# Optimization experiments

Hardware: AMD Instinct MI355X
Metric: run time of the kernel (lower is better)

Reference implementation:

```python
import jax, jax.numpy as jnp
import numpy as np

# Model constants (match init_kwargs config)
D_MODEL, D_INNER, D_HEAD, N_HEADS = 1024, 2048, 64, 32
D_STATE, D_CONV, CHUNK, N_LAYERS = 64, 4, 256, 2
CONV_DIM = D_INNER + 2 * D_STATE        # n_groups = 1
D_IN_PROJ = 2 * D_INNER + 2 * D_STATE + N_HEADS
B_SZ, L_SEQ = 2, 4096
EPS = 1e-5


def setup_inputs() -> dict:
    key = jax.random.key(0)
    ks = jax.random.split(key, 8)
    x = jax.random.normal(ks[0], (B_SZ, L_SEQ, D_MODEL), jnp.float32)
    in_proj_w = jax.random.normal(ks[1], (N_LAYERS, D_IN_PROJ, D_MODEL), jnp.float32) * 0.02
    conv_w = jax.random.normal(ks[2], (N_LAYERS, CONV_DIM, D_CONV), jnp.float32) * 0.2
    conv_b = jax.random.normal(ks[3], (N_LAYERS, CONV_DIM), jnp.float32) * 0.02
    # dt_bias init as in the torch code: inverse-softplus of dt ~ LogUniform(1e-3, 1e-1)
    dt = jnp.exp(jax.random.uniform(ks[4], (N_LAYERS, N_HEADS))
                 * (np.log(0.1) - np.log(0.001)) + np.log(0.001))
    dt = jnp.clip(dt, 1e-4, None)
    dt_bias = dt + jnp.log(-jnp.expm1(-dt))
    A_log = jnp.log(jax.random.uniform(ks[5], (N_LAYERS, N_HEADS), minval=1.0, maxval=16.0))
    D = jnp.ones((N_LAYERS, N_HEADS), jnp.float32)
    gnorm_w = jnp.ones((N_LAYERS, D_INNER), jnp.float32)
    out_proj_w = jax.random.normal(ks[6], (N_LAYERS, D_MODEL, D_INNER), jnp.float32) * 0.02
    norm_w = jnp.ones((N_LAYERS, D_MODEL), jnp.float32)
    return dict(x=x, in_proj_w=in_proj_w, conv_w=conv_w, conv_b=conv_b, dt_bias=dt_bias,
                A_log=A_log, D=D, gnorm_w=gnorm_w, out_proj_w=out_proj_w, norm_w=norm_w)


def _rmsnorm(x, w, eps=EPS):
    return x * jax.lax.rsqrt(jnp.mean(x * x, axis=-1, keepdims=True) + eps) * w


def _segsum(x):
    # x: (..., T) -> (..., T, T) with S[i, j] = sum_{j < k <= i} x[k], -inf above diag
    T = x.shape[-1]
    cs = jnp.cumsum(x, axis=-1)
    d = cs[..., :, None] - cs[..., None, :]
    return jnp.where(jnp.tril(jnp.ones((T, T), bool)), d, -jnp.inf)


def _causal_conv1d(x, w, b):
    # depthwise causal conv: x (B,L,C), w (C,K), b (C)
    K = w.shape[-1]
    L = x.shape[1]
    xp = jnp.pad(x, ((0, 0), (K - 1, 0), (0, 0)))
    out = jnp.broadcast_to(b, x.shape)
    for i in range(K):
        out = out + xp[:, i:i + L, :] * w[:, i]
    return out


def _ssd(X, dt, A, B, C, D):
    # Exact chunked SSD scan (mamba_chunk_scan_combined), n_groups=1.
    # X (b,l,h,p), dt (b,l,h), A (h), B,C (b,l,n)
    b, l, h, p = X.shape
    n = B.shape[-1]
    nc = l // CHUNK
    Xdt = X * dt[..., None]
    dA = (dt * A).reshape(b, nc, CHUNK, h).transpose(0, 3, 1, 2)     # (b,h,z,c)
    dAcs = jnp.cumsum(dA, axis=-1)
    Lmat = jnp.exp(_segsum(dA))                                      # (b,h,z,c,c)
    Bc = B.reshape(b, nc, CHUNK, n)
    Cc = C.reshape(b, nc, CHUNK, n)
    Xc = Xdt.reshape(b, nc, CHUNK, h, p)
    # intra-chunk (diagonal) part
    G = jnp.einsum('bzln,bzsn->bzls', Cc, Bc)                        # (b,z,c,c)
    M = G[:, None] * Lmat                                            # (b,h,z,c,c)
    Yd = jnp.einsum('bhzls,bzshp->bzlhp', M, Xc)
    # chunk states
    decay_states = jnp.exp(dAcs[..., -1:] - dAcs)                    # (b,h,z,c)
    states = jnp.einsum('bzln,bhzl,bzlhp->bzhpn', Bc, decay_states, Xc)
    # inter-chunk recurrence
    chunk_decay = jnp.exp(_segsum(jnp.pad(dAcs[..., -1], ((0, 0), (0, 0), (1, 0)))))
    states0 = jnp.concatenate([jnp.zeros_like(states[:, :1]), states], axis=1)
    prev = jnp.einsum('bhzc,bchpn->bzhpn', chunk_decay, states0)[:, :-1]
    Yo = jnp.einsum('bzln,bzhpn,bhzl->bzlhp', Cc, prev, jnp.exp(dAcs))
    Y = (Yd + Yo).reshape(b, l, h, p) + X * D[None, None, :, None]
    return Y


def _block(x, in_w, cw, cb, dtb, a_log, d_skip, gw, ow, nw):
    b, l, _ = x.shape
    h = _rmsnorm(x, nw)
    zxbcdt = jnp.einsum('bld,ed->ble', h, in_w)
    z = zxbcdt[..., :D_INNER]
    xBC = zxbcdt[..., D_INNER:D_INNER + CONV_DIM]
    dt = jax.nn.softplus(zxbcdt[..., D_INNER + CONV_DIM:] + dtb)      # (b,l,H)
    xBC = jax.nn.silu(_causal_conv1d(xBC, cw, cb))
    xs = xBC[..., :D_INNER].reshape(b, l, N_HEADS, D_HEAD)
    Bm = xBC[..., D_INNER:D_INNER + D_STATE]
    Cm = xBC[..., D_INNER + D_STATE:]
    A = -jnp.exp(a_log)
    y = _ssd(xs, dt, A, Bm, Cm, d_skip).reshape(b, l, D_INNER)
    y = _rmsnorm(y * jax.nn.silu(z), gw)                              # gated RMSNorm (gate before norm)
    return x + jnp.einsum('bli,di->bld', y, ow)


def reference(x, in_proj_w, conv_w, conv_b, dt_bias, A_log, D, gnorm_w, out_proj_w, norm_w):
    for i in range(in_proj_w.shape[0]):
        x = _block(x, in_proj_w[i], conv_w[i], conv_b[i], dt_bias[i],
                   A_log[i], D[i], gnorm_w[i], out_proj_w[i], norm_w[i])
    return x
```

## Files before the change

kernel.cpp:

```cpp
#include <hip/hip_runtime.h>

#define DMODEL   1024
#define DINNER   2048
#define NHEADS   32
#define DHEAD    64
#define DSTATE   64
#define CONVDIM  2176
#define DINPROJ  4256
#define LSEQ     4096
#define BSZ      2
#define NCHUNK   16
#define CHUNK    256
#define NROWS    8192
#define NPAD     4352
#define XT_P     264
#define M_P      40

typedef __attribute__((ext_vector_type(8))) short  short8;
typedef __attribute__((ext_vector_type(4))) float  f32x4;
typedef __attribute__((ext_vector_type(4))) unsigned short us4;

__device__ __forceinline__ float bf2f(unsigned short u){
  return __uint_as_float(((unsigned int)u) << 16);
}
__device__ __forceinline__ unsigned short f2bf(float f){
  unsigned int i = __float_as_uint(f);
  i += 0x7fffu + ((i >> 16) & 1u);
  return (unsigned short)(i >> 16);
}

__device__ __forceinline__ void gl_lds16(const void* g, void* l){
  __builtin_amdgcn_global_load_lds(
      (const __attribute__((address_space(1))) unsigned int*)g,
      (__attribute__((address_space(3))) unsigned int*)l, 16, 0, 0);
}

__global__ void cast_pad_kernel(const float* __restrict__ src, unsigned short* __restrict__ dst,
                                int rows_src, int cols, long long total){
  long long i = (long long)blockIdx.x * 256 + threadIdx.x;
  if (i >= total) return;
  long long r = i / cols;
  dst[i] = (r < rows_src) ? f2bf(src[i]) : (unsigned short)0;
}

__global__ void rmsnorm_kernel(const float* __restrict__ x, const float* __restrict__ w,
                               unsigned short* __restrict__ out){
  int r = blockIdx.x, t = threadIdx.x;
  const float* xr = x + (size_t)r * DMODEL;
  float v[4]; float s = 0.f;
#pragma unroll
  for (int i = 0; i < 4; ++i){ v[i] = xr[t + i*256]; s += v[i]*v[i]; }
  __shared__ float red[4];
  for (int off = 32; off; off >>= 1) s += __shfl_down(s, off, 64);
  if ((t & 63) == 0) red[t >> 6] = s;
  __syncthreads();
  s = red[0] + red[1] + red[2] + red[3];
  float sc = rsqrtf(s * (1.f/DMODEL) + 1e-5f);
#pragma unroll
  for (int i = 0; i < 4; ++i)
    out[(size_t)r*DMODEL + t + i*256] = f2bf(v[i]*sc*w[t + i*256]);
}

template<int EPI>
__launch_bounds__(256, 2)
__global__ void gemm_bt(const unsigned short* __restrict__ A, const unsigned short* __restrict__ Bw,
                        void* __restrict__ Cout, const float* __restrict__ Cres,
                        int K, int Nstore){
  __shared__ __align__(16) unsigned short As[128*64];
  __shared__ __align__(16) unsigned short Bs[128*64];
  const int m0 = blockIdx.y * 128, n0 = blockIdx.x * 128;
  const int t = threadIdx.x, w = t >> 6, lane = t & 63;
  const int wr = w >> 1, wc = w & 1;
  const int srow = lane >> 3;
  const int scol = (lane & 7) * 8;
  f32x4 acc[4][4] = {};

  for (int k0 = 0; k0 < K; k0 += 64){
#pragma unroll
    for (int it = 0; it < 4; ++it){
      int rr = (w*4 + it)*8 + srow;
      gl_lds16(A  + (size_t)(m0 + rr)*K + k0 + scol, &As[(w*4 + it)*512]);
      gl_lds16(Bw + (size_t)(n0 + rr)*K + k0 + scol, &Bs[(w*4 + it)*512]);
    }
    __syncthreads();
#pragma unroll
    for (int kk = 0; kk < 64; kk += 32){
      short8 af[4], bfr[4];
      int col = kk + (lane >> 4)*8;
#pragma unroll
      for (int m = 0; m < 4; ++m)
        af[m] = *(const short8*)&As[(wr*64 + m*16 + (lane & 15))*64 + col];
#pragma unroll
      for (int n = 0; n < 4; ++n)
        bfr[n] = *(const short8*)&Bs[(wc*64 + n*16 + (lane & 15))*64 + col];
#pragma unroll
      for (int m = 0; m < 4; ++m)
#pragma unroll
        for (int n = 0; n < 4; ++n)
          acc[m][n] = __builtin_amdgcn_mfma_f32_16x16x32_bf16(af[m], bfr[n], acc[m][n], 0, 0, 0);
    }
    __syncthreads();
  }

#pragma unroll
  for (int m = 0; m < 4; ++m){
#pragma unroll
    for (int n = 0; n < 4; ++n){
      int col = n0 + wc*64 + n*16 + (lane & 15);
      if (col < Nstore){
#pragma unroll
        for (int r = 0; r < 4; ++r){
          int row = m0 + wr*64 + m*16 + (lane >> 4)*4 + r;
          if (EPI == 0)
            ((unsigned short*)Cout)[(size_t)row*Nstore + col] = f2bf(acc[m][n][r]);
          else
            ((float*)Cout)[(size_t)row*Nstore + col] =
                Cres[(size_t)row*Nstore + col] + acc[m][n][r];
        }
      }
    }
  }
}

__global__ void conv_silu_kernel(const unsigned short* __restrict__ zx,
                                 const float* __restrict__ cw, const float* __restrict__ cb,
                                 unsigned short* __restrict__ X, unsigned short* __restrict__ Bm,
                                 unsigned short* __restrict__ Cm){
  int c = blockIdx.x * 256 + threadIdx.x;
  if (c >= CONVDIM) return;
  int r = blockIdx.y;
  int l = r & (LSEQ - 1);
  float acc = cb[c];
  float w0 = cw[c*4+0], w1 = cw[c*4+1], w2 = cw[c*4+2], w3 = cw[c*4+3];
#pragma unroll
  for (int i = 0; i < 4; ++i){
    int li = l - 3 + i;
    if (li >= 0){
      float v = bf2f(zx[(size_t)(r - 3 + i)*DINPROJ + DINNER + c]);
      float wi = (i==0)?w0:(i==1)?w1:(i==2)?w2:w3;
      acc += v * wi;
    }
  }
  float s = acc / (1.f + __expf(-acc));
  if (c < DINNER)            X[(size_t)r*DINNER + c]        = f2bf(s);
  else if (c < DINNER+DSTATE) Bm[(size_t)r*DSTATE + c-DINNER] = f2bf(s);
  else                        Cm[(size_t)r*DSTATE + c-DINNER-DSTATE] = f2bf(s);
}

__global__ void dtscan_kernel(const unsigned short* __restrict__ zx, const float* __restrict__ dtb,
                              const float* __restrict__ A_log,
                              float* __restrict__ dt_sp, float* __restrict__ dAcs_g){
  const int z = blockIdx.x, hh = blockIdx.y, b = blockIdx.z;
  const int t = threadIdx.x;
  __shared__ float sdA[CHUNK];
  const float Ah = -__expf(A_log[hh]);
  size_t r = (size_t)b*LSEQ + z*CHUNK + t;
  float raw = bf2f(zx[r*DINPROJ + DINNER + CONVDIM + hh]) + dtb[hh];
  float dtv = raw > 20.f ? raw : log1pf(__expf(raw));
  sdA[t] = dtv * Ah;
  __syncthreads();
  for (int off = 1; off < CHUNK; off <<= 1){
    float v = (t >= off) ? sdA[t - off] : 0.f;
    __syncthreads();
    sdA[t] += v;
    __syncthreads();
  }
  size_t hb = (size_t)(b*NHEADS + hh);
  dt_sp[hb*LSEQ + z*CHUNK + t] = dtv;
  dAcs_g[(hb*NCHUNK + z)*CHUNK + t] = sdA[t];
}

__launch_bounds__(256, 2)
__global__ void chunk_main_kernel(const unsigned short* __restrict__ X,
                                  const unsigned short* __restrict__ Bm,
                                  const unsigned short* __restrict__ Cm,
                                  const float* __restrict__ dt_sp,
                                  const float* __restrict__ dAcs_g,
                                  float* __restrict__ states,
                                  unsigned short* __restrict__ Yb){
  const int z = blockIdx.x, hh = blockIdx.y, b = blockIdx.z;
  const int t = threadIdx.x, w = t >> 6, lane = t & 63;
  __shared__ __align__(16) unsigned short Xt[64 * XT_P];
  __shared__ __align__(16) unsigned short U[64 * XT_P];
  __shared__ float sdA[CHUNK];
  __shared__ float sdt[CHUNK];

  const size_t row0 = (size_t)b*LSEQ + z*CHUNK;
  const size_t hb = (size_t)(b*NHEADS + hh);
  sdA[t] = dAcs_g[(hb*NCHUNK + z)*CHUNK + t];
  sdt[t] = dt_sp[hb*LSEQ + z*CHUNK + t];
  __syncthreads();
  const float total = sdA[CHUNK-1];

  for (int it = 0; it < 16; ++it){
    int l = it*16 + (t >> 4);
    int p4 = (t & 15) * 4;
    float dtl = sdt[l];
    float dec = __expf(total - sdA[l]);
    us4 xv = *(const us4*)(X  + (row0 + l)*DINNER + hh*DHEAD + p4);
    us4 bv = *(const us4*)(Bm + (row0 + l)*DSTATE + p4);
#pragma unroll
    for (int j = 0; j < 4; ++j){
      Xt[(p4 + j)*XT_P + l] = f2bf(bf2f(xv[j]) * dtl);
      U [(p4 + j)*XT_P + l] = f2bf(bf2f(bv[j]) * dec);
    }
  }
  __syncthreads();

  {
    f32x4 sacc[4] = {};
    for (int k2 = 0; k2 < 8; ++k2){
      int kc = k2*32 + (lane >> 4)*8;
      short8 a = *(const short8*)&U[(w*16 + (lane & 15))*XT_P + kc];
#pragma unroll
      for (int pt = 0; pt < 4; ++pt){
        short8 bfr = *(const short8*)&Xt[(pt*16 + (lane & 15))*XT_P + kc];
        sacc[pt] = __builtin_amdgcn_mfma_f32_16x16x32_bf16(a, bfr, sacc[pt], 0, 0, 0);
      }
    }
    float* sp = states + (((size_t)b*NCHUNK + z)*NHEADS + hh)*(DHEAD*DSTATE);
#pragma unroll
    for (int pt = 0; pt < 4; ++pt){
      int p = pt*16 + (lane & 15);
#pragma unroll
      for (int r = 0; r < 4; ++r){
        int n = w*16 + (lane >> 4)*4 + r;
        sp[p*DSTATE + n] = sacc[pt][r];
      }
    }
  }
  __syncthreads();

  unsigned short* Mw = U + w * (64 * M_P);
  short8 cfr[4][2];
#pragma unroll
  for (int lt = 0; lt < 4; ++lt){
    int lg = w + lt*4;
#pragma unroll
    for (int k2 = 0; k2 < 2; ++k2)
      cfr[lt][k2] = *(const short8*)(Cm + (row0 + lg*16 + (lane & 15))*DSTATE + k2*32 + (lane >> 4)*8);
  }
  f32x4 yacc[4][4] = {};
  for (int st = 0; st < 8; ++st){
    short8 gb[2][2];
#pragma unroll
    for (int ss = 0; ss < 2; ++ss)
#pragma unroll
      for (int k2 = 0; k2 < 2; ++k2)
        gb[ss][k2] = *(const short8*)(Bm + (row0 + st*32 + ss*16 + (lane & 15))*DSTATE + k2*32 + (lane >> 4)*8);
    short8 xb[4];
#pragma unroll
    for (int pt = 0; pt < 4; ++pt)
      xb[pt] = *(const short8*)&Xt[(pt*16 + (lane & 15))*XT_P + st*32 + (lane >> 4)*8];
#pragma unroll
    for (int lt = 0; lt < 4; ++lt){
      int lg = w + lt*4;
      if (st*32 > lg*16 + 15) continue;
#pragma unroll
      for (int ss = 0; ss < 2; ++ss){
        f32x4 g = {};
        g = __builtin_amdgcn_mfma_f32_16x16x32_bf16(cfr[lt][0], gb[ss][0], g, 0, 0, 0);
        g = __builtin_amdgcn_mfma_f32_16x16x32_bf16(cfr[lt][1], gb[ss][1], g, 0, 0, 0);
        int s = st*32 + ss*16 + (lane & 15);
        float sdAs = sdA[s];
#pragma unroll
        for (int r = 0; r < 4; ++r){
          int l = lg*16 + (lane >> 4)*4 + r;
          float m = (s <= l) ? __expf(sdA[l] - sdAs) : 0.f;
          Mw[(lt*16 + (lane >> 4)*4 + r)*M_P + ss*16 + (lane & 15)] = f2bf(g[r] * m);
        }
      }
      short8 mf = *(const short8*)&Mw[(lt*16 + (lane & 15))*M_P + (lane >> 4)*8];
#pragma unroll
      for (int pt = 0; pt < 4; ++pt)
        yacc[lt][pt] = __builtin_amdgcn_mfma_f32_16x16x32_bf16(mf, xb[pt], yacc[lt][pt], 0, 0, 0);
    }
  }
  __syncthreads();

  unsigned short* Yst = U + w * 4096;
#pragma unroll
  for (int lt = 0; lt < 4; ++lt)
#pragma unroll
    for (int pt = 0; pt < 4; ++pt)
#pragma unroll
      for (int r = 0; r < 4; ++r){
        int row = lt*16 + (lane >> 4)*4 + r;
        int c = pt*16 + (lane & 15);
        int cs = (c & 7) | ((((c >> 3) ^ (row & 7)) & 7) << 3);
        Yst[row*64 + cs] = f2bf(yacc[lt][pt][r]);
      }
  __syncthreads();
  {
    int ltl = lane >> 4, rr = lane & 15;
    int row = ltl*16 + rr;
    int lg = (w + ltl*4)*16 + rr;
    unsigned short* dst = Yb + (row0 + lg)*DINNER + hh*DHEAD;
#pragma unroll
    for (int k = 0; k < 8; ++k){
      short8 v = *(const short8*)&Yst[row*64 + ((k ^ (row & 7)) << 3)];
      *(short8*)(dst + k*8) = v;
    }
  }
}

__launch_bounds__(64)
__global__ void state_recur_kernel(const float* __restrict__ states, const float* __restrict__ dAcs_g,
                                   unsigned short* __restrict__ prev_bf){
  const int hh = blockIdx.x, b = blockIdx.y, t = threadIdx.x;
  float S[64];
#pragma unroll
  for (int j = 0; j < 64; ++j) S[j] = 0.f;
  for (int z = 0; z < NCHUNK; ++z){
    size_t idx = (((size_t)b*NCHUNK + z)*NHEADS + hh)*(DHEAD*DSTATE) + (size_t)t*DSTATE;
    float cd = __expf(dAcs_g[(((size_t)(b*NHEADS + hh))*NCHUNK + z)*CHUNK + CHUNK-1]);
    const float* st = states + idx;
    unsigned short* pb = prev_bf + idx;
#pragma unroll
    for (int j = 0; j < 64; ++j){
      pb[j] = f2bf(S[j]);
      S[j] = S[j]*cd + st[j];
    }
  }
}

__launch_bounds__(256, 2)
__global__ void chunk_out_kernel(const unsigned short* __restrict__ X,
                                 const unsigned short* __restrict__ Cm,
                                 const float* __restrict__ dAcs_g, const unsigned short* __restrict__ prev_bf,
                                 const float* __restrict__ Dp, unsigned short* __restrict__ Yb){
  const int z = blockIdx.x, hh = blockIdx.y, b = blockIdx.z;
  const int t = threadIdx.x, w = t >> 6, lane = t & 63;
  __shared__ __align__(16) float Yo[4][64*64];
  __shared__ float sdA[CHUNK];
  const size_t row0 = (size_t)b*LSEQ + z*CHUNK;
  sdA[t] = dAcs_g[(((size_t)(b*NHEADS + hh))*NCHUNK + z)*CHUNK + t];
  __syncthreads();
  const unsigned short* pvb = prev_bf + (((size_t)b*NCHUNK + z)*NHEADS + hh)*(DHEAD*DSTATE);
  const float Dh = Dp[hh];

  f32x4 acc[4][4] = {};
#pragma unroll
  for (int k2 = 0; k2 < 2; ++k2){
    int kc = k2*32 + (lane >> 4)*8;
    short8 a[4], bfr[4];
#pragma unroll
    for (int lt = 0; lt < 4; ++lt)
      a[lt] = *(const short8*)(Cm + (row0 + w*64 + lt*16 + (lane & 15))*DSTATE + kc);
#pragma unroll
    for (int pt = 0; pt < 4; ++pt)
      bfr[pt] = *(const short8*)(pvb + (size_t)(pt*16 + (lane & 15))*DSTATE + kc);
#pragma unroll
    for (int lt = 0; lt < 4; ++lt)
#pragma unroll
      for (int pt = 0; pt < 4; ++pt)
        acc[lt][pt] = __builtin_amdgcn_mfma_f32_16x16x32_bf16(a[lt], bfr[pt], acc[lt][pt], 0, 0, 0);
  }

#pragma unroll
  for (int lt = 0; lt < 4; ++lt){
    float eA[4];
#pragma unroll
    for (int r = 0; r < 4; ++r)
      eA[r] = __expf(sdA[w*64 + lt*16 + (lane >> 4)*4 + r]);
#pragma unroll
    for (int pt = 0; pt < 4; ++pt){
      int c = pt*16 + (lane & 15);
#pragma unroll
      for (int r = 0; r < 4; ++r){
        int row = lt*16 + (lane >> 4)*4 + r;
        int blk = ((c >> 2) ^ (row & 15)) & 15;
        Yo[w][row*64 + (c & 3) + (blk << 2)] = acc[lt][pt][r] * eA[r];
      }
    }
  }
  __syncthreads();
  {
    int l = w*64 + lane;
    const unsigned short* xr = X + (row0 + l)*DINNER + hh*DHEAD;
    unsigned short* yr = Yb + (row0 + l)*DINNER + hh*DHEAD;
#pragma unroll
    for (int k = 0; k < 16; ++k){
      f32x4 v = *(const f32x4*)&Yo[w][lane*64 + (((k ^ (lane & 15)) & 15) << 2)];
      us4 yb = *(const us4*)(yr + k*4);
      us4 xv = *(const us4*)(xr + k*4);
      us4 o;
#pragma unroll
      for (int j = 0; j < 4; ++j)
        o[j] = f2bf(bf2f(yb[j]) + v[j] + Dh*bf2f(xv[j]));
      *(us4*)(yr + k*4) = o;
    }
  }
}

__global__ void gated_rmsnorm_kernel(const unsigned short* __restrict__ Yb,
                                     const unsigned short* __restrict__ zx,
                                     const float* __restrict__ gw, unsigned short* __restrict__ out){
  int r = blockIdx.x, t = threadIdx.x;
  float vals[8]; float s = 0.f;
#pragma unroll
  for (int i = 0; i < 8; ++i){
    int c = t + i*256;
    float y  = bf2f(Yb[(size_t)r*DINNER + c]);
    float zv = bf2f(zx[(size_t)r*DINPROJ + c]);
    float g  = y * (zv / (1.f + __expf(-zv)));
    vals[i] = g; s += g*g;
  }
  __shared__ float red[4];
  for (int off = 32; off; off >>= 1) s += __shfl_down(s, off, 64);
  if ((t & 63) == 0) red[t >> 6] = s;
  __syncthreads();
  s = red[0] + red[1] + red[2] + red[3];
  float sc = rsqrtf(s * (1.f/DINNER) + 1e-5f);
#pragma unroll
  for (int i = 0; i < 8; ++i)
    out[(size_t)r*DINNER + t + i*256] = f2bf(vals[i]*sc*gw[t + i*256]);
}

extern "C" void kernel_launch(void* const* d_in, const int* in_sizes, int n_in,
                              void* d_out, int out_size, void* d_ws, size_t ws_size,
                              hipStream_t stream){
  const float* x      = (const float*)d_in[0];
  const float* in_w   = (const float*)d_in[1];
  const float* conv_w = (const float*)d_in[2];
  const float* conv_b = (const float*)d_in[3];
  const float* dt_b   = (const float*)d_in[4];
  const float* A_log  = (const float*)d_in[5];
  const float* Dp     = (const float*)d_in[6];
  const float* gnw    = (const float*)d_in[7];
  const float* out_w  = (const float*)d_in[8];
  const float* norm_w = (const float*)d_in[9];
  float* outp = (float*)d_out;

  const size_t NEEDED =
      (size_t)NROWS*DMODEL*2 + (size_t)NPAD*DMODEL*2 + (size_t)DMODEL*DINNER*2
    + (size_t)NROWS*DINPROJ*2 + (size_t)NROWS*DINNER*2  + (size_t)NROWS*DINNER*2
    + (size_t)NROWS*DSTATE*2*2 + (size_t)BSZ*NHEADS*LSEQ*4
    + (size_t)BSZ*NHEADS*NCHUNK*CHUNK*4
    + (size_t)BSZ*NCHUNK*NHEADS*DHEAD*DSTATE*4
    + (size_t)BSZ*NCHUNK*NHEADS*DHEAD*DSTATE*2
    + 40*256;
  if (ws_size < NEEDED) return;

  char* p = (char*)d_ws;
  auto alloc = [&](size_t n){ char* r = p; p += (n + 255) & ~(size_t)255; return (void*)r; };
  unsigned short* h    = (unsigned short*)alloc((size_t)NROWS*DMODEL*2);
  unsigned short* wA   = (unsigned short*)alloc((size_t)NPAD*DMODEL*2);
  unsigned short* wO   = (unsigned short*)alloc((size_t)DMODEL*DINNER*2);
  unsigned short* zx   = (unsigned short*)alloc((size_t)NROWS*DINPROJ*2);
  unsigned short* X    = (unsigned short*)alloc((size_t)NROWS*DINNER*2);
  unsigned short* Yb   = (unsigned short*)alloc((size_t)NROWS*DINNER*2);
  unsigned short* Bm   = (unsigned short*)alloc((size_t)NROWS*DSTATE*2);
  unsigned short* Cm   = (unsigned short*)alloc((size_t)NROWS*DSTATE*2);
  float* dtbuf  = (float*)alloc((size_t)BSZ*NHEADS*LSEQ*4);
  float* dAcs   = (float*)alloc((size_t)BSZ*NHEADS*NCHUNK*CHUNK*4);
  float* states = (float*)alloc((size_t)BSZ*NCHUNK*NHEADS*DHEAD*DSTATE*4);
  unsigned short* prev_bf = (unsigned short*)alloc((size_t)BSZ*NCHUNK*NHEADS*DHEAD*DSTATE*2);
  unsigned short* yn = X;

  for (int layer = 0; layer < 2; ++layer){
    const float* xprev = (layer == 0) ? x : outp;
    float* xnext = outp;

    cast_pad_kernel<<<(NPAD*DMODEL + 255)/256, 256, 0, stream>>>(
        in_w + (size_t)layer*DINPROJ*DMODEL, wA, DINPROJ, DMODEL, (long long)NPAD*DMODEL);
    rmsnorm_kernel<<<NROWS, 256, 0, stream>>>(xprev, norm_w + layer*DMODEL, h);
    gemm_bt<0><<<dim3(NPAD/128, NROWS/128), 256, 0, stream>>>(
        h, wA, (void*)zx, nullptr, DMODEL, DINPROJ);
    conv_silu_kernel<<<dim3((CONVDIM + 255)/256, NROWS), 256, 0, stream>>>(
        zx, conv_w + (size_t)layer*CONVDIM*4, conv_b + layer*CONVDIM, X, Bm, Cm);
    dtscan_kernel<<<dim3(NCHUNK, NHEADS, BSZ), 256, 0, stream>>>(
        zx, dt_b + layer*NHEADS, A_log + layer*NHEADS, dtbuf, dAcs);
    chunk_main_kernel<<<dim3(NCHUNK, NHEADS, BSZ), 256, 0, stream>>>(
        X, Bm, Cm, dtbuf, dAcs, states, Yb);
    state_recur_kernel<<<dim3(NHEADS, BSZ), 64, 0, stream>>>(states, dAcs, prev_bf);
    chunk_out_kernel<<<dim3(NCHUNK, NHEADS, BSZ), 256, 0, stream>>>(
        X, Cm, dAcs, prev_bf, Dp + layer*NHEADS, Yb);
    gated_rmsnorm_kernel<<<NROWS, 256, 0, stream>>>(Yb, zx, gnw + layer*DINNER, yn);
    cast_pad_kernel<<<(DMODEL*DINNER + 255)/256, 256, 0, stream>>>(
        out_w + (size_t)layer*DMODEL*DINNER, wO, DMODEL, DINNER, (long long)DMODEL*DINNER);
    gemm_bt<1><<<dim3(DMODEL/128, NROWS/128), 256, 0, stream>>>(
        yn, wO, (void*)xnext, xprev, DINNER, DMODEL);
  }
  (void)in_sizes; (void)n_in; (void)out_size;
}
```

Measured before the change: 795.9 us.

## Use 256x256-tile GEMM with 4-stage LDS pipeline for in_proj

Adds a new bf16 GEMM kernel with 256x256 output tiles, 512 threads and a 4-deep ring of K=32 LDS buffers. Global loads are prefetched three tiles ahead and gated with explicit vmcnt waits. It also uses an XOR-swizzled LDS layout and remaps workgroup IDs across XCDs. The in_proj GEMM now uses this kernel to get more reuse per tile and better overlap of loads with MFMA work, at the cost of fewer workgroups (544) and one block per CU.

After: 862.8 us. 1.08x slower.

```diff
diff --git a/kernel.cpp b/kernel.cpp
--- a/kernel.cpp
+++ b/kernel.cpp
@@ -62,6 +62,88 @@
 }
 
 template<int EPI>
+__launch_bounds__(512, 1)
+__global__ void gemm256_bt(const unsigned short* __restrict__ A, const unsigned short* __restrict__ Bw,
+                           void* __restrict__ Cout, const float* __restrict__ Cres,
+                           int K, int Nstore, int nbx){
+  __shared__ __align__(16) unsigned short As[4][256*32];
+  __shared__ __align__(16) unsigned short Bs[4][256*32];
+  const int nwg = gridDim.x;
+  int id = blockIdx.x;
+  if ((nwg & 7) == 0) id = (id & 7)*(nwg >> 3) + (id >> 3);
+  const int m0 = (id / nbx) * 256, n0 = (id % nbx) * 256;
+  const int tid = threadIdx.x, w = tid >> 6, lane = tid & 63;
+  const int wr = w >> 2, wc = w & 3;
+  const int nt = K >> 5;
+
+  const int rQ = lane >> 2;
+  const int bQ = (lane & 3) ^ (rQ & 3);
+  const int koff = ((lane >> 4) ^ (lane & 3)) * 8;
+
+  auto STAGE = [&](int bufi, int tile){
+    const int k0 = tile << 5;
+#pragma unroll
+    for (int i = 0; i < 2; ++i){
+      int r = w*32 + i*16 + rQ;
+      gl_lds16(A  + (size_t)(m0 + r)*K + k0 + bQ*8, &As[bufi][(w*32 + i*16)*32]);
+      gl_lds16(Bw + (size_t)(n0 + r)*K + k0 + bQ*8, &Bs[bufi][(w*32 + i*16)*32]);
+    }
+  };
+
+  f32x4 acc[8][4] = {};
+  STAGE(0, 0); STAGE(1, 1); STAGE(2, 2);
+
+  for (int t = 0; t < nt; ++t){
+    if (t < nt-2)       asm volatile("s_waitcnt vmcnt(8)" ::: "memory");
+    else if (t == nt-2) asm volatile("s_waitcnt vmcnt(4)" ::: "memory");
+    else                asm volatile("s_waitcnt vmcnt(0)" ::: "memory");
+    __builtin_amdgcn_s_barrier();
+    asm volatile("" ::: "memory");
+    if (t + 3 < nt) STAGE((t+3)&3, t+3);
+
+    const unsigned short* Ab = As[t&3];
+    const unsigned short* Bb = Bs[t&3];
+    short8 af[8], bv[4];
+#pragma unroll
+    for (int mf = 0; mf < 8; ++mf)
+      af[mf] = *(const short8*)&Ab[(wr*128 + mf*16 + (lane & 15))*32 + koff];
+#pragma unroll
+    for (int nf = 0; nf < 4; ++nf)
+      bv[nf] = *(const short8*)&Bb[(wc*64 + nf*16 + (lane & 15))*32 + koff];
+    asm volatile("s_waitcnt lgkmcnt(0)" ::: "memory");
+    __builtin_amdgcn_sched_barrier(0);
+    __builtin_amdgcn_s_setprio(1);
+#pragma unroll
+    for (int mf = 0; mf < 8; ++mf)
+#pragma unroll
+      for (int nf = 0; nf < 4; ++nf)
+        acc[mf][nf] = __builtin_amdgcn_mfma_f32_16x16x32_bf16(af[mf], bv[nf], acc[mf][nf], 0, 0, 0);
+    __builtin_amdgcn_s_setprio(0);
+    asm volatile("" ::: "memory");
+    __builtin_amdgcn_s_barrier();
+  }
+
+#pragma unroll
+  for (int mf = 0; mf < 8; ++mf){
+#pragma unroll
+    for (int nf = 0; nf < 4; ++nf){
+      int col = n0 + wc*64 + nf*16 + (lane & 15);
+      if (col < Nstore){
+#pragma unroll
+        for (int r = 0; r < 4; ++r){
+          int row = m0 + wr*128 + mf*16 + (lane >> 4)*4 + r;
+          if (EPI == 0)
+            ((unsigned short*)Cout)[(size_t)row*Nstore + col] = f2bf(acc[mf][nf][r]);
+          else
+            ((float*)Cout)[(size_t)row*Nstore + col] =
+                Cres[(size_t)row*Nstore + col] + acc[mf][nf][r];
+        }
+      }
+    }
+  }
+}
+
+template<int EPI>
 __launch_bounds__(256, 2)
 __global__ void gemm_bt(const unsigned short* __restrict__ A, const unsigned short* __restrict__ Bw,
                         void* __restrict__ Cout, const float* __restrict__ Cres,
@@ -465,8 +547,8 @@
     cast_pad_kernel<<<(NPAD*DMODEL + 255)/256, 256, 0, stream>>>(
         in_w + (size_t)layer*DINPROJ*DMODEL, wA, DINPROJ, DMODEL, (long long)NPAD*DMODEL);
     rmsnorm_kernel<<<NROWS, 256, 0, stream>>>(xprev, norm_w + layer*DMODEL, h);
-    gemm_bt<0><<<dim3(NPAD/128, NROWS/128), 256, 0, stream>>>(
-        h, wA, (void*)zx, nullptr, DMODEL, DINPROJ);
+    gemm256_bt<0><<<dim3((NROWS/256)*(NPAD/256)), 512, 0, stream>>>(
+        h, wA, (void*)zx, nullptr, DMODEL, DINPROJ, NPAD/256);
     conv_silu_kernel<<<dim3((CONVDIM + 255)/256, NROWS), 256, 0, stream>>>(
         zx, conv_w + (size_t)layer*CONVDIM*4, conv_b + layer*CONVDIM, X, Bm, Cm);
     dtscan_kernel<<<dim3(NCHUNK, NHEADS, BSZ), 256, 0, stream>>>(
```
